# Performance work log

Hardware: AMD Instinct MI355X
Metric: run time of the kernel (lower is better)

## Reference

```python
import jax, jax.numpy as jnp
from jax import lax
import numpy as np

B, N, J, NI, D = 2, 2048, 24, 9, 3
CD, HID = 16, 128
SOFT_BLEND = 20.0
MAX_STEPS, CVG = 50, 1e-5
INIT_BONES = np.array([0, 1, 2, 4, 5, 16, 17, 18, 19])


def _mlp(params, x):
    h = x
    for W, b in params[:-1]:
        h = jax.nn.softplus(h @ W + b)
    W, b = params[-1]
    return h @ W + b


def _broyden(g, x0, J_inv0):
    # x0: [P,3,1], J_inv0: [P,3,3]; fixed MAX_STEPS iterations, track best iterate
    gx = g(x0)
    err0 = jnp.linalg.norm(gx, axis=(1, 2))
    state = (x0, gx, J_inv0, -(J_inv0 @ gx), x0, err0)

    def body(i, st):
        x, gx, Jinv, upd, bx, berr = st
        dx = upd
        x = x + dx
        gx_new = g(x)
        dgx = gx_new - gx
        vT = jnp.swapaxes(dx, -2, -1) @ Jinv            # [P,1,3]
        a = dx - Jinv @ dgx                              # [P,3,1]
        b = vT @ dgx + 1e-6                              # [P,1,1]
        Jinv = Jinv + (a / b) @ vT                       # rank-1 Broyden update
        upd = -(Jinv @ gx_new)
        err = jnp.linalg.norm(gx_new, axis=(1, 2))
        better = err < berr
        bx = jnp.where(better[:, None, None], x, bx)
        berr = jnp.where(better, err, berr)
        return (x, gx_new, Jinv, upd, bx, berr)

    st = lax.fori_loop(0, MAX_STEPS, body, state)
    return st[4], st[5] < CVG


def setup_inputs():
    key = jax.random.key(0)
    ks = jax.random.split(key, 24)
    xd = 0.5 * jax.random.normal(ks[0], (B, N, D), jnp.float32)
    cond_latent = jax.random.normal(ks[1], (B, CD), jnp.float32)
    # near-identity invertible bone transforms
    R = jnp.eye(3, dtype=jnp.float32) + 0.1 * jax.random.normal(ks[2], (B, J, 3, 3), jnp.float32)
    t = 0.1 * jax.random.normal(ks[3], (B, J, 3), jnp.float32)
    tfs = jnp.zeros((B, J, 4, 4), jnp.float32)
    tfs = tfs.at[..., :3, :3].set(R).at[..., :3, 3].set(t).at[..., 3, 3].set(1.0)

    def w(k, fi, fo):
        return jax.random.normal(k, (fi, fo), jnp.float32) / np.sqrt(fi)

    din = D + CD
    inp = dict(xd=xd, cond_latent=cond_latent, tfs=tfs)
    dims_lbs = [(din, HID), (HID, HID), (HID, HID), (HID, J)]
    dims_disp = [(din, HID), (HID, HID), (HID, HID), (HID, D)]
    for i, (fi, fo) in enumerate(dims_lbs):
        inp[f"lbs_w{i}"] = w(ks[4 + i], fi, fo)
        inp[f"lbs_b{i}"] = jnp.zeros((fo,), jnp.float32)
    for i, (fi, fo) in enumerate(dims_disp):
        inp[f"disp_w{i}"] = w(ks[10 + i], fi, fo)
        inp[f"disp_b{i}"] = jnp.zeros((fo,), jnp.float32)
    return inp


def _forward(xd, cond_latent, tfs, lbs, disp):
    P = B * N
    xd_f = xd.reshape(P, D)
    cond_f = jnp.broadcast_to(cond_latent[:, None], (B, N, CD)).reshape(P, CD)
    tfs_f = jnp.broadcast_to(tfs[:, None], (B, N, J, 4, 4)).reshape(P, J, 4, 4)

    # __init: inverse-skin xd with one-hot weights at each init bone -> [P, NI, 3]
    xd_h = jnp.concatenate([xd_f, jnp.ones((P, 1), xd.dtype)], -1)
    xc_init = jnp.einsum('pnij,pj->pni', jnp.linalg.inv(tfs_f[:, INIT_BONES]), xd_h)[..., :3]

    PI = P * NI
    cond_e = jnp.repeat(cond_f, NI, axis=0)       # [PI, CD]
    tfs_e = jnp.repeat(tfs_f, NI, axis=0)         # [PI, J, 4, 4]
    xd_tgt = jnp.repeat(xd_f, NI, axis=0)         # [PI, 3]
    x0 = xc_init.reshape(PI, D)

    def fwd_skin(xc, lbs_p, cond_p, tfs_p):
        w = jax.nn.softmax(SOFT_BLEND * _mlp(lbs_p, jnp.concatenate([xc, cond_p], -1)), -1)
        xh = jnp.concatenate([xc, jnp.ones_like(xc[:, :1])], -1)
        return jnp.einsum('pn,pnij,pj->pi', w, tfs_p, xh)[:, :3]

    def fwd_skin_pt(x, c, t, lbs_p):
        w = jax.nn.softmax(SOFT_BLEND * _mlp(lbs_p, jnp.concatenate([x, c])))
        xh = jnp.concatenate([x, jnp.ones((1,), x.dtype)])
        return jnp.einsum('n,nij,j->i', w, t, xh)[:3]

    def gradient(xc, lbs_p, cond_p, tfs_p):
        # per-point 3x3 Jacobian of forward skinning wrt canonical point
        f = lambda x, c, t: fwd_skin_pt(x, c, t, lbs_p)
        return jax.vmap(jax.jacfwd(f), in_axes=(0, 0, 0))(xc, cond_p, tfs_p)

    # stop-gradient copies for the no-grad broyden search (torch.no_grad block)
    sg = lax.stop_gradient
    lbs_sg = [(sg(W), sg(b)) for W, b in lbs]
    cond_sg, tfs_sg, xdt_sg = sg(cond_e), sg(tfs_e), sg(xd_tgt)

    J_inv0 = jnp.linalg.inv(gradient(sg(x0), lbs_sg, cond_sg, tfs_sg))

    def g_ng(x):  # x: [PI,3,1]
        return (fwd_skin(x[..., 0], lbs_sg, cond_sg, tfs_sg) - xdt_sg)[..., None]

    x_opt, valid = _broyden(g_ng, sg(x0)[..., None], J_inv0)
    xc_opt = sg(x_opt[..., 0])

    # implicit-differentiation correction (eval_mode=False path)
    xd_opt = fwd_skin(xc_opt, lbs, cond_e, tfs_e)
    grad_inv = jnp.linalg.inv(gradient(xc_opt, lbs, cond_e, tfs_e))
    corr = jnp.einsum('pij,pj->pi', -sg(grad_inv), xd_opt - sg(xd_opt))
    xc = xc_opt + corr

    # __query_cano: beta displacement network
    xc = xc + _mlp(disp, jnp.concatenate([xc, cond_e], -1))
    return xc.reshape(B, N, NI, D), valid.reshape(B, N, NI)


def reference(xd, cond_latent, tfs, lbs_w0, lbs_b0, lbs_w1, lbs_b1, lbs_w2, lbs_b2, lbs_w3, lbs_b3, disp_w0, disp_b0, disp_w1, disp_b1, disp_w2, disp_b2, disp_w3, disp_b3):
    lbs = [(lbs_w0, lbs_b0), (lbs_w1, lbs_b1), (lbs_w2, lbs_b2), (lbs_w3, lbs_b3)]
    disp = [(disp_w0, disp_b0), (disp_w1, disp_b1), (disp_w2, disp_b2), (disp_w3, disp_b3)]
    return _forward(xd, cond_latent, tfs, lbs, disp)
```

## Files before the change

### kernel.cpp

```cpp
#include <hip/hip_runtime.h>
#include <hip/hip_bf16.h>
#include <math.h>

#define NB 2
#define NN 2048
#define NJ 24
#define NIB 9
#define NCD 16
#define NHID 128
#define NP (NB * NN)
#define NPI (NP * NIB)
#define NBSTRIDE (NN * NIB)
#define SBLEND 20.0f
#define CVG_EPS 1e-5f
#define MAX_STEPS 50

#define HSTR 129
#define INSTRD 21
#define LSTR 25

static __device__ __forceinline__ float softplusf(float x) {
    return fmaxf(x, 0.0f) + log1pf(expf(-fabsf(x)));
}
static __device__ __forceinline__ float sigmoidf(float x) {
    return 1.0f / (1.0f + expf(-x));
}
static __device__ __forceinline__ int bone_of(int ib) {
    return (ib < 3) ? ib : ((ib < 5) ? ib + 1 : ib + 11);
}

template <int K>
static __device__ __forceinline__ void mv_acc32(const float* __restrict__ Wp, const float* inrow,
                                                int jb, float* acc) {
#pragma unroll 4
    for (int k = 0; k < K; k++) {
        float h = inrow[k];
        const float* wk = Wp + k * NHID + jb;
#pragma unroll
        for (int jj = 0; jj < 32; jj++) acc[jj] = fmaf(h, wk[jj], acc[jj]);
    }
}

template <int K, int LDIN>
static __device__ __forceinline__ void val_layer(const float* __restrict__ Wp,
                                                 const float* __restrict__ bp,
                                                 const float* inbase, float (*Hs)[HSTR], int r,
                                                 int jb, bool prebar) {
    float acc[32];
#pragma unroll
    for (int jj = 0; jj < 32; jj++) acc[jj] = bp[jb + jj];
    mv_acc32<K>(Wp, inbase + r * LDIN, jb, acc);
    if (prebar) __syncthreads();
#pragma unroll
    for (int jj = 0; jj < 32; jj++) Hs[r][jb + jj] = softplusf(acc[jj]);
    __syncthreads();
}

template <int K, int LDIN>
static __device__ __forceinline__ void jac_layer(const float* __restrict__ Wp,
                                                 const float* __restrict__ bp,
                                                 const float* inbase, float (*Hs)[HSTR], int r,
                                                 int jb, bool prebar) {
    const bool isval = (r < 16);
    const int p = r & 15;
    float acc[32];
#pragma unroll
    for (int jj = 0; jj < 32; jj++) acc[jj] = isval ? bp[jb + jj] : 0.0f;
    mv_acc32<K>(Wp, inbase + r * LDIN, jb, acc);
    if (prebar) __syncthreads();
#pragma unroll
    for (int jj = 0; jj < 32; jj++) Hs[r][jb + jj] = acc[jj];
    __syncthreads();
    float zv[32];
    if (!isval) {
#pragma unroll
        for (int jj = 0; jj < 32; jj++) zv[jj] = Hs[p][jb + jj];
    }
    __syncthreads();
    if (isval) {
#pragma unroll
        for (int jj = 0; jj < 32; jj++) Hs[r][jb + jj] = softplusf(acc[jj]);
    } else {
#pragma unroll
        for (int jj = 0; jj < 32; jj++) Hs[r][jb + jj] = sigmoidf(zv[jj]) * acc[jj];
    }
    __syncthreads();
}

template <int NC, int LDW, bool JAC>
static __device__ __forceinline__ void logit_layer(const float* __restrict__ Wp,
                                                   const float* __restrict__ bp,
                                                   const float* inbase, float (*Lgs)[LSTR], int r,
                                                   int wid) {
    const int jb = wid * NC;
    const bool isval = (!JAC) || (r < 16);
    float acc[NC];
#pragma unroll
    for (int jj = 0; jj < NC; jj++) acc[jj] = isval ? bp[jb + jj] : 0.0f;
#pragma unroll 4
    for (int k = 0; k < NHID; k++) {
        float h = inbase[r * HSTR + k];
        const float* wk = Wp + k * LDW + jb;
#pragma unroll
        for (int jj = 0; jj < NC; jj++) acc[jj] = fmaf(h, wk[jj], acc[jj]);
    }
#pragma unroll
    for (int jj = 0; jj < NC; jj++) Lgs[r][jb + jj] = acc[jj];
    __syncthreads();
}

__global__ __launch_bounds__(256) void kernel_fused(
    const float* __restrict__ xd, const float* __restrict__ cond, const float* __restrict__ tfs,
    const float* __restrict__ lw0, const float* __restrict__ lb0,
    const float* __restrict__ lw1, const float* __restrict__ lb1,
    const float* __restrict__ lw2, const float* __restrict__ lb2,
    const float* __restrict__ lw3, const float* __restrict__ lb3,
    const float* __restrict__ dw0, const float* __restrict__ db0,
    const float* __restrict__ dw1, const float* __restrict__ db1,
    const float* __restrict__ dw2, const float* __restrict__ db2,
    const float* __restrict__ dw3, const float* __restrict__ db3,
    float* __restrict__ out) {
    __shared__ float sIN[64][INSTRD];
    __shared__ float sH[64][HSTR];
    __shared__ float sLg[64][LSTR];
    __shared__ float sTm[NJ * 12];
    __shared__ int sFlag;

    const int tid = threadIdx.x;
    const int r = tid & 63;
    const int wid = __builtin_amdgcn_readfirstlane(tid >> 6);
    const int jb = wid * 32;
    const int pi0 = blockIdx.x * 64;
    const int b = pi0 / NBSTRIDE;
    const int pi = pi0 + r;

    for (int t = tid; t < NJ * 12; t += 256) {
        int j = t / 12, rc = t % 12;
        sTm[t] = tfs[(size_t)(b * NJ + j) * 16 + rc];
    }
    if (tid >= 16 && tid < 64) {
        const int d = (tid >> 4) - 1;
#pragma unroll
        for (int k = 0; k < 19; k++) sIN[tid][k] = (k == d) ? 1.0f : 0.0f;
    }
    if (tid < 16) {
#pragma unroll
        for (int cc = 0; cc < NCD; cc++) sIN[tid][3 + cc] = cond[b * NCD + cc];
    }

    float x0_ = 0, x1_ = 0, x2_ = 0, g0 = 0, g1 = 0, g2 = 0;
    float Ji0 = 0, Ji1 = 0, Ji2 = 0, Ji3 = 0, Ji4 = 0, Ji5 = 0, Ji6 = 0, Ji7 = 0, Ji8 = 0;
    float u0 = 0, u1 = 0, u2 = 0, bx0 = 0, bx1 = 0, bx2 = 0, berr = 0;
    float tx = 0, ty = 0, tz = 0;
    if (tid < 64) {
        const int pp = pi / NIB;
        tx = xd[pp * 3 + 0]; ty = xd[pp * 3 + 1]; tz = xd[pp * 3 + 2];
    }

#pragma unroll 1
    for (int pass = 0; pass < 4; ++pass) {
        __syncthreads();
        if ((tid >> 4) == pass) {
            const int p = tid & 15;
            const int ib = pi % NIB;
            const int bone = bone_of(ib);
            const float* T = tfs + (size_t)(b * NJ + bone) * 16;
            float r00 = T[0], r01 = T[1], r02 = T[2], t0 = T[3];
            float r10 = T[4], r11 = T[5], r12 = T[6], t1 = T[7];
            float r20 = T[8], r21 = T[9], r22 = T[10], t2 = T[11];
            float det = r00 * (r11 * r22 - r12 * r21) - r01 * (r10 * r22 - r12 * r20) +
                        r02 * (r10 * r21 - r11 * r20);
            float rd = 1.0f / det;
            float i00 = (r11 * r22 - r12 * r21) * rd, i01 = -(r01 * r22 - r02 * r21) * rd,
                  i02 = (r01 * r12 - r02 * r11) * rd;
            float i10 = -(r10 * r22 - r12 * r20) * rd, i11 = (r00 * r22 - r02 * r20) * rd,
                  i12 = -(r00 * r12 - r02 * r10) * rd;
            float i20 = (r10 * r21 - r11 * r20) * rd, i21 = -(r00 * r21 - r01 * r20) * rd,
                  i22 = (r00 * r11 - r01 * r10) * rd;
            float vx = tx - t0, vy = ty - t1, vz = tz - t2;
            x0_ = i00 * vx + i01 * vy + i02 * vz;
            x1_ = i10 * vx + i11 * vy + i12 * vz;
            x2_ = i20 * vx + i21 * vy + i22 * vz;
            sIN[p][0] = x0_; sIN[p][1] = x1_; sIN[p][2] = x2_;
        }
        __syncthreads();

        jac_layer<19, INSTRD>(lw0, lb0, &sIN[0][0], sH, r, jb, false);
        jac_layer<NHID, HSTR>(lw1, lb1, &sH[0][0], sH, r, jb, true);
        jac_layer<NHID, HSTR>(lw2, lb2, &sH[0][0], sH, r, jb, true);
        logit_layer<6, NJ, true>(lw3, lb3, &sH[0][0], sLg, r, wid);

        if ((tid >> 4) == pass) {
            const int p = tid & 15;
            float mx = -1e30f;
#pragma unroll
            for (int j = 0; j < NJ; j++) mx = fmaxf(mx, SBLEND * sLg[p][j]);
            float S = 0.0f;
#pragma unroll
            for (int j = 0; j < NJ; j++) S += expf(SBLEND * sLg[p][j] - mx);
            const float invS = 1.0f / S;
            float d0 = 0, d1 = 0, d2 = 0;
#pragma unroll
            for (int j = 0; j < NJ; j++) {
                float sj = expf(SBLEND * sLg[p][j] - mx) * invS;
                d0 += sj * (SBLEND * sLg[16 + p][j]);
                d1 += sj * (SBLEND * sLg[32 + p][j]);
                d2 += sj * (SBLEND * sLg[48 + p][j]);
            }
            float f0 = 0, f1 = 0, f2 = 0;
            float J00 = 0, J01 = 0, J02 = 0, J10 = 0, J11 = 0, J12 = 0, J20 = 0, J21 = 0,
                  J22 = 0;
#pragma unroll
            for (int j = 0; j < NJ; j++) {
                float sj = expf(SBLEND * sLg[p][j] - mx) * invS;
                float uj0 = SBLEND * sLg[16 + p][j], uj1 = SBLEND * sLg[32 + p][j],
                      uj2 = SBLEND * sLg[48 + p][j];
                float sd0 = sj * (uj0 - d0), sd1 = sj * (uj1 - d1), sd2 = sj * (uj2 - d2);
                const float* M = &sTm[j * 12];
                float y0 = M[0] * x0_ + M[1] * x1_ + M[2] * x2_ + M[3];
                float y1 = M[4] * x0_ + M[5] * x1_ + M[6] * x2_ + M[7];
                float y2 = M[8] * x0_ + M[9] * x1_ + M[10] * x2_ + M[11];
                f0 += sj * y0; f1 += sj * y1; f2 += sj * y2;
                J00 += sd0 * y0 + sj * M[0]; J01 += sd1 * y0 + sj * M[1]; J02 += sd2 * y0 + sj * M[2];
                J10 += sd0 * y1 + sj * M[4]; J11 += sd1 * y1 + sj * M[5]; J12 += sd2 * y1 + sj * M[6];
                J20 += sd0 * y2 + sj * M[8]; J21 += sd1 * y2 + sj * M[9]; J22 += sd2 * y2 + sj * M[10];
            }
            g0 = f0 - tx; g1 = f1 - ty; g2 = f2 - tz;
            float detJ = J00 * (J11 * J22 - J12 * J21) - J01 * (J10 * J22 - J12 * J20) +
                         J02 * (J10 * J21 - J11 * J20);
            float rdJ = 1.0f / detJ;
            Ji0 = (J11 * J22 - J12 * J21) * rdJ; Ji1 = -(J01 * J22 - J02 * J21) * rdJ;
            Ji2 = (J01 * J12 - J02 * J11) * rdJ;
            Ji3 = -(J10 * J22 - J12 * J20) * rdJ; Ji4 = (J00 * J22 - J02 * J20) * rdJ;
            Ji5 = -(J00 * J12 - J02 * J10) * rdJ;
            Ji6 = (J10 * J21 - J11 * J20) * rdJ; Ji7 = -(J00 * J21 - J01 * J20) * rdJ;
            Ji8 = (J00 * J11 - J01 * J10) * rdJ;
            u0 = -(Ji0 * g0 + Ji1 * g1 + Ji2 * g2);
            u1 = -(Ji3 * g0 + Ji4 * g1 + Ji5 * g2);
            u2 = -(Ji6 * g0 + Ji7 * g1 + Ji8 * g2);
            berr = sqrtf(g0 * g0 + g1 * g1 + g2 * g2);
            bx0 = x0_; bx1 = x1_; bx2 = x2_;
        }
    }

    if (tid < 64) {
#pragma unroll
        for (int cc = 0; cc < NCD; cc++) sIN[tid][3 + cc] = cond[b * NCD + cc];
    }

#pragma unroll 1
    for (int it = 0; it < MAX_STEPS; ++it) {
        float dx0 = 0, dx1 = 0, dx2 = 0;
        if (tid < 64) {
            dx0 = u0; dx1 = u1; dx2 = u2;
            x0_ += dx0; x1_ += dx1; x2_ += dx2;
            sIN[tid][0] = x0_; sIN[tid][1] = x1_; sIN[tid][2] = x2_;
        }
        __syncthreads();

        val_layer<19, INSTRD>(lw0, lb0, &sIN[0][0], sH, r, jb, false);
        val_layer<NHID, HSTR>(lw1, lb1, &sH[0][0], sH, r, jb, true);
        val_layer<NHID, HSTR>(lw2, lb2, &sH[0][0], sH, r, jb, true);
        logit_layer<6, NJ, false>(lw3, lb3, &sH[0][0], sLg, r, wid);

        if (tid < 64) {
            float mx = -1e30f;
#pragma unroll
            for (int j = 0; j < NJ; j++) mx = fmaxf(mx, SBLEND * sLg[r][j]);
            float S = 0.0f;
#pragma unroll
            for (int j = 0; j < NJ; j++) {
                float e = expf(SBLEND * sLg[r][j] - mx);
                sLg[r][j] = e;
                S += e;
            }
            const float invS = 1.0f / S;
            float f0 = 0, f1 = 0, f2 = 0;
#pragma unroll
            for (int j = 0; j < NJ; j++) {
                float sj = sLg[r][j] * invS;
                const float* M = &sTm[j * 12];
                f0 += sj * (M[0] * x0_ + M[1] * x1_ + M[2] * x2_ + M[3]);
                f1 += sj * (M[4] * x0_ + M[5] * x1_ + M[6] * x2_ + M[7]);
                f2 += sj * (M[8] * x0_ + M[9] * x1_ + M[10] * x2_ + M[11]);
            }
            float gn0 = f0 - tx, gn1 = f1 - ty, gn2 = f2 - tz;
            float dg0 = gn0 - g0, dg1 = gn1 - g1, dg2 = gn2 - g2;
            float Jd0 = Ji0 * dg0 + Ji1 * dg1 + Ji2 * dg2;
            float Jd1 = Ji3 * dg0 + Ji4 * dg1 + Ji5 * dg2;
            float Jd2 = Ji6 * dg0 + Ji7 * dg1 + Ji8 * dg2;
            float v0 = dx0 * Ji0 + dx1 * Ji3 + dx2 * Ji6;
            float v1 = dx0 * Ji1 + dx1 * Ji4 + dx2 * Ji7;
            float v2 = dx0 * Ji2 + dx1 * Ji5 + dx2 * Ji8;
            float a0 = dx0 - Jd0, a1 = dx1 - Jd1, a2 = dx2 - Jd2;
            float bden = v0 * dg0 + v1 * dg1 + v2 * dg2 + 1e-6f;
            float s0 = a0 / bden, s1 = a1 / bden, s2 = a2 / bden;
            Ji0 += s0 * v0; Ji1 += s0 * v1; Ji2 += s0 * v2;
            Ji3 += s1 * v0; Ji4 += s1 * v1; Ji5 += s1 * v2;
            Ji6 += s2 * v0; Ji7 += s2 * v1; Ji8 += s2 * v2;
            u0 = -(Ji0 * gn0 + Ji1 * gn1 + Ji2 * gn2);
            u1 = -(Ji3 * gn0 + Ji4 * gn1 + Ji5 * gn2);
            u2 = -(Ji6 * gn0 + Ji7 * gn1 + Ji8 * gn2);
            float err = sqrtf(gn0 * gn0 + gn1 * gn1 + gn2 * gn2);
            if (err < berr) { berr = err; bx0 = x0_; bx1 = x1_; bx2 = x2_; }
            g0 = gn0; g1 = gn1; g2 = gn2;
            int allc = __all(berr < CVG_EPS);
            if (tid == 0) sFlag = allc;
        }
        __syncthreads();
        if (sFlag) break;
    }

    if (tid < 64) {
        sIN[tid][0] = bx0; sIN[tid][1] = bx1; sIN[tid][2] = bx2;
    }
    __syncthreads();

    val_layer<19, INSTRD>(dw0, db0, &sIN[0][0], sH, r, jb, false);
    val_layer<NHID, HSTR>(dw1, db1, &sH[0][0], sH, r, jb, true);
    val_layer<NHID, HSTR>(dw2, db2, &sH[0][0], sH, r, jb, true);

    if (tid < 64) {
        float a0 = db3[0], a1 = db3[1], a2 = db3[2];
#pragma unroll 4
        for (int k = 0; k < NHID; k++) {
            float h = sH[tid][k];
            a0 = fmaf(h, dw3[k * 3 + 0], a0);
            a1 = fmaf(h, dw3[k * 3 + 1], a1);
            a2 = fmaf(h, dw3[k * 3 + 2], a2);
        }
        out[pi * 3 + 0] = bx0 + a0;
        out[pi * 3 + 1] = bx1 + a1;
        out[pi * 3 + 2] = bx2 + a2;
        out[3 * NPI + pi] = (berr < CVG_EPS) ? 1.0f : 0.0f;
    }
}

extern "C" void kernel_launch(void* const* d_in, const int* in_sizes, int n_in,
                              void* d_out, int out_size, void* d_ws, size_t ws_size,
                              hipStream_t stream) {
    (void)in_sizes; (void)n_in; (void)out_size; (void)d_ws; (void)ws_size;
    const float* xd   = (const float*)d_in[0];
    const float* cond = (const float*)d_in[1];
    const float* tfs  = (const float*)d_in[2];
    const float* lw0 = (const float*)d_in[3];  const float* lb0 = (const float*)d_in[4];
    const float* lw1 = (const float*)d_in[5];  const float* lb1 = (const float*)d_in[6];
    const float* lw2 = (const float*)d_in[7];  const float* lb2 = (const float*)d_in[8];
    const float* lw3 = (const float*)d_in[9];  const float* lb3 = (const float*)d_in[10];
    const float* dw0 = (const float*)d_in[11]; const float* db0 = (const float*)d_in[12];
    const float* dw1 = (const float*)d_in[13]; const float* db1 = (const float*)d_in[14];
    const float* dw2 = (const float*)d_in[15]; const float* db2 = (const float*)d_in[16];
    const float* dw3 = (const float*)d_in[17]; const float* db3 = (const float*)d_in[18];
    float* out = (float*)d_out;

    kernel_fused<<<NPI / 64, 256, 0, stream>>>(xd, cond, tfs, lw0, lb0, lw1, lb1, lw2, lb2,
                                               lw3, lb3, dw0, db0, dw1, db1, dw2, db2, dw3, db3,
                                               out);
}
```

Before: 1.499 ms.

## Split Broyden solve into block pass plus compacted straggler pass

Splits the fused kernel into three launches. The first runs Broyden per 64-row block with 512 threads and exits early once at most 16 rows remain unconverged. It then writes the solver state of unconverged rows into a compacted workspace list through an atomic counter. A second kernel packs those stragglers densely and finishes their remaining iterations, and a third kernel runs the displacement MLP. This aims to stop whole blocks from iterating for a few slow rows and to double the threads per block, at the cost of workspace traffic, extra launches and a memset.

New measurement: 1.247 ms. 16.8% less time.

```diff
diff --git a/kernel.cpp b/kernel.cpp
--- a/kernel.cpp
+++ b/kernel.cpp
@@ -1,5 +1,4 @@
 #include <hip/hip_runtime.h>
-#include <hip/hip_bf16.h>
 #include <math.h>
 
 #define NB 2
@@ -14,11 +13,17 @@
 #define SBLEND 20.0f
 #define CVG_EPS 1e-5f
 #define MAX_STEPS 50
+#define THRESH 16
 
 #define HSTR 129
 #define INSTRD 21
 #define LSTR 25
 
+#define WS_BX 4
+#define WS_BE (4 + 3 * NPI)
+#define WS_META (4 + 4 * NPI)
+#define WS_ST (4 + 5 * NPI)
+
 static __device__ __forceinline__ float softplusf(float x) {
     return fmaxf(x, 0.0f) + log1pf(expf(-fabsf(x)));
 }
@@ -30,14 +35,14 @@
 }
 
 template <int K>
-static __device__ __forceinline__ void mv_acc32(const float* __restrict__ Wp, const float* inrow,
+static __device__ __forceinline__ void mv_acc16(const float* __restrict__ Wp, const float* inrow,
                                                 int jb, float* acc) {
 #pragma unroll 4
     for (int k = 0; k < K; k++) {
         float h = inrow[k];
         const float* wk = Wp + k * NHID + jb;
 #pragma unroll
-        for (int jj = 0; jj < 32; jj++) acc[jj] = fmaf(h, wk[jj], acc[jj]);
+        for (int jj = 0; jj < 16; jj++) acc[jj] = fmaf(h, wk[jj], acc[jj]);
     }
 }
 
@@ -46,13 +51,13 @@
                                                  const float* __restrict__ bp,
                                                  const float* inbase, float (*Hs)[HSTR], int r,
                                                  int jb, bool prebar) {
-    float acc[32];
-#pragma unroll
-    for (int jj = 0; jj < 32; jj++) acc[jj] = bp[jb + jj];
-    mv_acc32<K>(Wp, inbase + r * LDIN, jb, acc);
+    float acc[16];
+#pragma unroll
+    for (int jj = 0; jj < 16; jj++) acc[jj] = bp[jb + jj];
+    mv_acc16<K>(Wp, inbase + r * LDIN, jb, acc);
     if (prebar) __syncthreads();
 #pragma unroll
-    for (int jj = 0; jj < 32; jj++) Hs[r][jb + jj] = softplusf(acc[jj]);
+    for (int jj = 0; jj < 16; jj++) Hs[r][jb + jj] = softplusf(acc[jj]);
     __syncthreads();
 }
 
@@ -63,78 +68,124 @@
                                                  int jb, bool prebar) {
     const bool isval = (r < 16);
     const int p = r & 15;
-    float acc[32];
-#pragma unroll
-    for (int jj = 0; jj < 32; jj++) acc[jj] = isval ? bp[jb + jj] : 0.0f;
-    mv_acc32<K>(Wp, inbase + r * LDIN, jb, acc);
+    float acc[16];
+#pragma unroll
+    for (int jj = 0; jj < 16; jj++) acc[jj] = isval ? bp[jb + jj] : 0.0f;
+    mv_acc16<K>(Wp, inbase + r * LDIN, jb, acc);
     if (prebar) __syncthreads();
 #pragma unroll
-    for (int jj = 0; jj < 32; jj++) Hs[r][jb + jj] = acc[jj];
+    for (int jj = 0; jj < 16; jj++) Hs[r][jb + jj] = acc[jj];
     __syncthreads();
-    float zv[32];
+    float zv[16];
     if (!isval) {
 #pragma unroll
-        for (int jj = 0; jj < 32; jj++) zv[jj] = Hs[p][jb + jj];
+        for (int jj = 0; jj < 16; jj++) zv[jj] = Hs[p][jb + jj];
     }
     __syncthreads();
     if (isval) {
 #pragma unroll
-        for (int jj = 0; jj < 32; jj++) Hs[r][jb + jj] = softplusf(acc[jj]);
+        for (int jj = 0; jj < 16; jj++) Hs[r][jb + jj] = softplusf(acc[jj]);
     } else {
 #pragma unroll
-        for (int jj = 0; jj < 32; jj++) Hs[r][jb + jj] = sigmoidf(zv[jj]) * acc[jj];
+        for (int jj = 0; jj < 16; jj++) Hs[r][jb + jj] = sigmoidf(zv[jj]) * acc[jj];
     }
     __syncthreads();
 }
 
-template <int NC, int LDW, bool JAC>
+template <bool JAC>
 static __device__ __forceinline__ void logit_layer(const float* __restrict__ Wp,
                                                    const float* __restrict__ bp,
                                                    const float* inbase, float (*Lgs)[LSTR], int r,
                                                    int wid) {
-    const int jb = wid * NC;
+    const int jb = wid * 3;
     const bool isval = (!JAC) || (r < 16);
-    float acc[NC];
-#pragma unroll
-    for (int jj = 0; jj < NC; jj++) acc[jj] = isval ? bp[jb + jj] : 0.0f;
+    float acc[3];
+#pragma unroll
+    for (int jj = 0; jj < 3; jj++) acc[jj] = isval ? bp[jb + jj] : 0.0f;
 #pragma unroll 4
     for (int k = 0; k < NHID; k++) {
         float h = inbase[r * HSTR + k];
-        const float* wk = Wp + k * LDW + jb;
-#pragma unroll
-        for (int jj = 0; jj < NC; jj++) acc[jj] = fmaf(h, wk[jj], acc[jj]);
-    }
-#pragma unroll
-    for (int jj = 0; jj < NC; jj++) Lgs[r][jb + jj] = acc[jj];
+        const float* wk = Wp + k * NJ + jb;
+#pragma unroll
+        for (int jj = 0; jj < 3; jj++) acc[jj] = fmaf(h, wk[jj], acc[jj]);
+    }
+#pragma unroll
+    for (int jj = 0; jj < 3; jj++) Lgs[r][jb + jj] = acc[jj];
     __syncthreads();
 }
 
-__global__ __launch_bounds__(256) void kernel_fused(
+static __device__ __forceinline__ void broyden_step(
+    float* sLgRow, const float* sTm, float tx, float ty, float tz,
+    float dx0, float dx1, float dx2,
+    float& x0_, float& x1_, float& x2_, float& g0, float& g1, float& g2,
+    float& Ji0, float& Ji1, float& Ji2, float& Ji3, float& Ji4, float& Ji5,
+    float& Ji6, float& Ji7, float& Ji8,
+    float& u0, float& u1, float& u2,
+    float& bx0, float& bx1, float& bx2, float& berr) {
+    float mx = -1e30f;
+#pragma unroll
+    for (int j = 0; j < NJ; j++) mx = fmaxf(mx, SBLEND * sLgRow[j]);
+    float S = 0.0f;
+#pragma unroll
+    for (int j = 0; j < NJ; j++) {
+        float e = expf(SBLEND * sLgRow[j] - mx);
+        sLgRow[j] = e;
+        S += e;
+    }
+    const float invS = 1.0f / S;
+    float f0 = 0, f1 = 0, f2 = 0;
+#pragma unroll
+    for (int j = 0; j < NJ; j++) {
+        float sj = sLgRow[j] * invS;
+        const float* M = &sTm[j * 12];
+        f0 += sj * (M[0] * x0_ + M[1] * x1_ + M[2] * x2_ + M[3]);
+        f1 += sj * (M[4] * x0_ + M[5] * x1_ + M[6] * x2_ + M[7]);
+        f2 += sj * (M[8] * x0_ + M[9] * x1_ + M[10] * x2_ + M[11]);
+    }
+    float gn0 = f0 - tx, gn1 = f1 - ty, gn2 = f2 - tz;
+    float dg0 = gn0 - g0, dg1 = gn1 - g1, dg2 = gn2 - g2;
+    float Jd0 = Ji0 * dg0 + Ji1 * dg1 + Ji2 * dg2;
+    float Jd1 = Ji3 * dg0 + Ji4 * dg1 + Ji5 * dg2;
+    float Jd2 = Ji6 * dg0 + Ji7 * dg1 + Ji8 * dg2;
+    float v0 = dx0 * Ji0 + dx1 * Ji3 + dx2 * Ji6;
+    float v1 = dx0 * Ji1 + dx1 * Ji4 + dx2 * Ji7;
+    float v2 = dx0 * Ji2 + dx1 * Ji5 + dx2 * Ji8;
+    float a0 = dx0 - Jd0, a1 = dx1 - Jd1, a2 = dx2 - Jd2;
+    float bden = v0 * dg0 + v1 * dg1 + v2 * dg2 + 1e-6f;
+    float s0 = a0 / bden, s1 = a1 / bden, s2 = a2 / bden;
+    Ji0 += s0 * v0; Ji1 += s0 * v1; Ji2 += s0 * v2;
+    Ji3 += s1 * v0; Ji4 += s1 * v1; Ji5 += s1 * v2;
+    Ji6 += s2 * v0; Ji7 += s2 * v1; Ji8 += s2 * v2;
+    u0 = -(Ji0 * gn0 + Ji1 * gn1 + Ji2 * gn2);
+    u1 = -(Ji3 * gn0 + Ji4 * gn1 + Ji5 * gn2);
+    u2 = -(Ji6 * gn0 + Ji7 * gn1 + Ji8 * gn2);
+    float err = sqrtf(gn0 * gn0 + gn1 * gn1 + gn2 * gn2);
+    if (err < berr) { berr = err; bx0 = x0_; bx1 = x1_; bx2 = x2_; }
+    g0 = gn0; g1 = gn1; g2 = gn2;
+}
+
+__global__ __launch_bounds__(512) void kernel_a(
     const float* __restrict__ xd, const float* __restrict__ cond, const float* __restrict__ tfs,
     const float* __restrict__ lw0, const float* __restrict__ lb0,
     const float* __restrict__ lw1, const float* __restrict__ lb1,
     const float* __restrict__ lw2, const float* __restrict__ lb2,
     const float* __restrict__ lw3, const float* __restrict__ lb3,
-    const float* __restrict__ dw0, const float* __restrict__ db0,
-    const float* __restrict__ dw1, const float* __restrict__ db1,
-    const float* __restrict__ dw2, const float* __restrict__ db2,
-    const float* __restrict__ dw3, const float* __restrict__ db3,
-    float* __restrict__ out) {
+    float* __restrict__ ws) {
     __shared__ float sIN[64][INSTRD];
     __shared__ float sH[64][HSTR];
     __shared__ float sLg[64][LSTR];
     __shared__ float sTm[NJ * 12];
-    __shared__ int sFlag;
+    __shared__ int sCnt;
 
     const int tid = threadIdx.x;
     const int r = tid & 63;
     const int wid = __builtin_amdgcn_readfirstlane(tid >> 6);
-    const int jb = wid * 32;
+    const int jb = wid * 16;
     const int pi0 = blockIdx.x * 64;
     const int b = pi0 / NBSTRIDE;
     const int pi = pi0 + r;
 
-    for (int t = tid; t < NJ * 12; t += 256) {
+    for (int t = tid; t < NJ * 12; t += 512) {
         int j = t / 12, rc = t % 12;
         sTm[t] = tfs[(size_t)(b * NJ + j) * 16 + rc];
     }
@@ -160,11 +211,10 @@
 #pragma unroll 1
     for (int pass = 0; pass < 4; ++pass) {
         __syncthreads();
-        if ((tid >> 4) == pass) {
+        if (tid < 64 && (tid >> 4) == pass) {
             const int p = tid & 15;
             const int ib = pi % NIB;
-            const int bone = bone_of(ib);
-            const float* T = tfs + (size_t)(b * NJ + bone) * 16;
+            const float* T = tfs + (size_t)(b * NJ + bone_of(ib)) * 16;
             float r00 = T[0], r01 = T[1], r02 = T[2], t0 = T[3];
             float r10 = T[4], r11 = T[5], r12 = T[6], t1 = T[7];
             float r20 = T[8], r21 = T[9], r22 = T[10], t2 = T[11];
@@ -188,9 +238,9 @@
         jac_layer<19, INSTRD>(lw0, lb0, &sIN[0][0], sH, r, jb, false);
         jac_layer<NHID, HSTR>(lw1, lb1, &sH[0][0], sH, r, jb, true);
         jac_layer<NHID, HSTR>(lw2, lb2, &sH[0][0], sH, r, jb, true);
-        logit_layer<6, NJ, true>(lw3, lb3, &sH[0][0], sLg, r, wid);
-
-        if ((tid >> 4) == pass) {
+        logit_layer<true>(lw3, lb3, &sH[0][0], sLg, r, wid);
+
+        if (tid < 64 && (tid >> 4) == pass) {
             const int p = tid & 15;
             float mx = -1e30f;
 #pragma unroll
@@ -248,6 +298,7 @@
         for (int cc = 0; cc < NCD; cc++) sIN[tid][3 + cc] = cond[b * NCD + cc];
     }
 
+    int itdone = MAX_STEPS;
 #pragma unroll 1
     for (int it = 0; it < MAX_STEPS; ++it) {
         float dx0 = 0, dx1 = 0, dx2 = 0;
@@ -261,58 +312,173 @@
         val_layer<19, INSTRD>(lw0, lb0, &sIN[0][0], sH, r, jb, false);
         val_layer<NHID, HSTR>(lw1, lb1, &sH[0][0], sH, r, jb, true);
         val_layer<NHID, HSTR>(lw2, lb2, &sH[0][0], sH, r, jb, true);
-        logit_layer<6, NJ, false>(lw3, lb3, &sH[0][0], sLg, r, wid);
+        logit_layer<false>(lw3, lb3, &sH[0][0], sLg, r, wid);
 
         if (tid < 64) {
-            float mx = -1e30f;
-#pragma unroll
-            for (int j = 0; j < NJ; j++) mx = fmaxf(mx, SBLEND * sLg[r][j]);
-            float S = 0.0f;
-#pragma unroll
-            for (int j = 0; j < NJ; j++) {
-                float e = expf(SBLEND * sLg[r][j] - mx);
-                sLg[r][j] = e;
-                S += e;
+            broyden_step(&sLg[r][0], sTm, tx, ty, tz, dx0, dx1, dx2,
+                         x0_, x1_, x2_, g0, g1, g2,
+                         Ji0, Ji1, Ji2, Ji3, Ji4, Ji5, Ji6, Ji7, Ji8,
+                         u0, u1, u2, bx0, bx1, bx2, berr);
+            unsigned long long m = __ballot(!(berr < CVG_EPS));
+            if (tid == 0) sCnt = (int)__popcll(m);
+        }
+        __syncthreads();
+        if (sCnt <= THRESH) { itdone = it + 1; break; }
+    }
+
+    if (tid < 64) {
+        ws[WS_BX + pi * 3 + 0] = bx0;
+        ws[WS_BX + pi * 3 + 1] = bx1;
+        ws[WS_BX + pi * 3 + 2] = bx2;
+        ws[WS_BE + pi] = berr;
+        const int remaining = MAX_STEPS - itdone;
+        if (remaining > 0 && !(berr < CVG_EPS)) {
+            int idx = atomicAdd((int*)ws + b, 1);
+            int slot = b * NBSTRIDE + idx;
+            ((int*)ws)[WS_META + slot] = pi | (remaining << 20);
+            float st[15] = {x0_, x1_, x2_, g0, g1, g2, Ji0, Ji1, Ji2, Ji3, Ji4, Ji5, Ji6, Ji7, Ji8};
+#pragma unroll
+            for (int c = 0; c < 15; c++) ws[WS_ST + c * NPI + slot] = st[c];
+        }
+    }
+}
+
+__global__ __launch_bounds__(512) void kernel_b(
+    const float* __restrict__ xd, const float* __restrict__ cond, const float* __restrict__ tfs,
+    const float* __restrict__ lw0, const float* __restrict__ lb0,
+    const float* __restrict__ lw1, const float* __restrict__ lb1,
+    const float* __restrict__ lw2, const float* __restrict__ lb2,
+    const float* __restrict__ lw3, const float* __restrict__ lb3,
+    float* __restrict__ ws) {
+    const int bid = blockIdx.x;
+    const int batch = (bid < 288) ? 0 : 1;
+    const int chunk0 = (bid - batch * 288) * 64;
+    const int S = ((const int*)ws)[batch];
+    if (chunk0 >= S) return;
+
+    __shared__ float sIN[64][INSTRD];
+    __shared__ float sH[64][HSTR];
+    __shared__ float sLg[64][LSTR];
+    __shared__ float sTm[NJ * 12];
+    __shared__ int sCnt;
+
+    const int tid = threadIdx.x;
+    const int r = tid & 63;
+    const int wid = __builtin_amdgcn_readfirstlane(tid >> 6);
+    const int jb = wid * 16;
+
+    for (int t = tid; t < NJ * 12; t += 512) {
+        int j = t / 12, rc = t % 12;
+        sTm[t] = tfs[(size_t)(batch * NJ + j) * 16 + rc];
+    }
+
+    float x0_ = 0, x1_ = 0, x2_ = 0, g0 = 0, g1 = 0, g2 = 0;
+    float Ji0 = 1, Ji1 = 0, Ji2 = 0, Ji3 = 0, Ji4 = 1, Ji5 = 0, Ji6 = 0, Ji7 = 0, Ji8 = 1;
+    float u0 = 0, u1 = 0, u2 = 0, bx0 = 0, bx1 = 0, bx2 = 0, berr = 0;
+    float tx = 0, ty = 0, tz = 0;
+    int pi = -1, itleft = 0;
+    bool realrow = false;
+    if (tid < 64) {
+        const int k = chunk0 + r;
+        realrow = (k < S);
+        if (realrow) {
+            const int slot = batch * NBSTRIDE + k;
+            const int meta = ((const int*)ws)[WS_META + slot];
+            pi = meta & 0xFFFFF;
+            itleft = meta >> 20;
+            x0_ = ws[WS_ST + 0 * NPI + slot]; x1_ = ws[WS_ST + 1 * NPI + slot];
+            x2_ = ws[WS_ST + 2 * NPI + slot];
+            g0 = ws[WS_ST + 3 * NPI + slot]; g1 = ws[WS_ST + 4 * NPI + slot];
+            g2 = ws[WS_ST + 5 * NPI + slot];
+            Ji0 = ws[WS_ST + 6 * NPI + slot]; Ji1 = ws[WS_ST + 7 * NPI + slot];
+            Ji2 = ws[WS_ST + 8 * NPI + slot];
+            Ji3 = ws[WS_ST + 9 * NPI + slot]; Ji4 = ws[WS_ST + 10 * NPI + slot];
+            Ji5 = ws[WS_ST + 11 * NPI + slot];
+            Ji6 = ws[WS_ST + 12 * NPI + slot]; Ji7 = ws[WS_ST + 13 * NPI + slot];
+            Ji8 = ws[WS_ST + 14 * NPI + slot];
+            u0 = -(Ji0 * g0 + Ji1 * g1 + Ji2 * g2);
+            u1 = -(Ji3 * g0 + Ji4 * g1 + Ji5 * g2);
+            u2 = -(Ji6 * g0 + Ji7 * g1 + Ji8 * g2);
+            bx0 = ws[WS_BX + pi * 3 + 0]; bx1 = ws[WS_BX + pi * 3 + 1];
+            bx2 = ws[WS_BX + pi * 3 + 2];
+            berr = ws[WS_BE + pi];
+            const int pp = pi / NIB;
+            tx = xd[pp * 3 + 0]; ty = xd[pp * 3 + 1]; tz = xd[pp * 3 + 2];
+        }
+#pragma unroll
+        for (int cc = 0; cc < NCD; cc++) sIN[tid][3 + cc] = cond[batch * NCD + cc];
+        sIN[tid][0] = 0; sIN[tid][1] = 0; sIN[tid][2] = 0;
+    }
+
+#pragma unroll 1
+    for (int it = 0; it < MAX_STEPS; ++it) {
+        bool active = false;
+        float dx0 = 0, dx1 = 0, dx2 = 0;
+        if (tid < 64) {
+            active = realrow && (itleft > 0) && !(berr < CVG_EPS);
+            if (active) {
+                dx0 = u0; dx1 = u1; dx2 = u2;
+                x0_ += dx0; x1_ += dx1; x2_ += dx2;
             }
-            const float invS = 1.0f / S;
-            float f0 = 0, f1 = 0, f2 = 0;
-#pragma unroll
-            for (int j = 0; j < NJ; j++) {
-                float sj = sLg[r][j] * invS;
-                const float* M = &sTm[j * 12];
-                f0 += sj * (M[0] * x0_ + M[1] * x1_ + M[2] * x2_ + M[3]);
-                f1 += sj * (M[4] * x0_ + M[5] * x1_ + M[6] * x2_ + M[7]);
-                f2 += sj * (M[8] * x0_ + M[9] * x1_ + M[10] * x2_ + M[11]);
+            sIN[tid][0] = x0_; sIN[tid][1] = x1_; sIN[tid][2] = x2_;
+        }
+        __syncthreads();
+
+        val_layer<19, INSTRD>(lw0, lb0, &sIN[0][0], sH, r, jb, false);
+        val_layer<NHID, HSTR>(lw1, lb1, &sH[0][0], sH, r, jb, true);
+        val_layer<NHID, HSTR>(lw2, lb2, &sH[0][0], sH, r, jb, true);
+        logit_layer<false>(lw3, lb3, &sH[0][0], sLg, r, wid);
+
+        if (tid < 64) {
+            if (active) {
+                broyden_step(&sLg[r][0], sTm, tx, ty, tz, dx0, dx1, dx2,
+                             x0_, x1_, x2_, g0, g1, g2,
+                             Ji0, Ji1, Ji2, Ji3, Ji4, Ji5, Ji6, Ji7, Ji8,
+                             u0, u1, u2, bx0, bx1, bx2, berr);
+                itleft--;
             }
-            float gn0 = f0 - tx, gn1 = f1 - ty, gn2 = f2 - tz;
-            float dg0 = gn0 - g0, dg1 = gn1 - g1, dg2 = gn2 - g2;
-            float Jd0 = Ji0 * dg0 + Ji1 * dg1 + Ji2 * dg2;
-            float Jd1 = Ji3 * dg0 + Ji4 * dg1 + Ji5 * dg2;
-            float Jd2 = Ji6 * dg0 + Ji7 * dg1 + Ji8 * dg2;
-            float v0 = dx0 * Ji0 + dx1 * Ji3 + dx2 * Ji6;
-            float v1 = dx0 * Ji1 + dx1 * Ji4 + dx2 * Ji7;
-            float v2 = dx0 * Ji2 + dx1 * Ji5 + dx2 * Ji8;
-            float a0 = dx0 - Jd0, a1 = dx1 - Jd1, a2 = dx2 - Jd2;
-            float bden = v0 * dg0 + v1 * dg1 + v2 * dg2 + 1e-6f;
-            float s0 = a0 / bden, s1 = a1 / bden, s2 = a2 / bden;
-            Ji0 += s0 * v0; Ji1 += s0 * v1; Ji2 += s0 * v2;
-            Ji3 += s1 * v0; Ji4 += s1 * v1; Ji5 += s1 * v2;
-            Ji6 += s2 * v0; Ji7 += s2 * v1; Ji8 += s2 * v2;
-            u0 = -(Ji0 * gn0 + Ji1 * gn1 + Ji2 * gn2);
-            u1 = -(Ji3 * gn0 + Ji4 * gn1 + Ji5 * gn2);
-            u2 = -(Ji6 * gn0 + Ji7 * gn1 + Ji8 * gn2);
-            float err = sqrtf(gn0 * gn0 + gn1 * gn1 + gn2 * gn2);
-            if (err < berr) { berr = err; bx0 = x0_; bx1 = x1_; bx2 = x2_; }
-            g0 = gn0; g1 = gn1; g2 = gn2;
-            int allc = __all(berr < CVG_EPS);
-            if (tid == 0) sFlag = allc;
+            unsigned long long m =
+                __ballot(realrow && (itleft > 0) && !(berr < CVG_EPS));
+            if (tid == 0) sCnt = (int)__popcll(m);
         }
         __syncthreads();
-        if (sFlag) break;
-    }
-
+        if (sCnt == 0) break;
+    }
+
+    if (tid < 64 && realrow) {
+        ws[WS_BX + pi * 3 + 0] = bx0;
+        ws[WS_BX + pi * 3 + 1] = bx1;
+        ws[WS_BX + pi * 3 + 2] = bx2;
+        ws[WS_BE + pi] = berr;
+    }
+}
+
+__global__ __launch_bounds__(512) void kernel_c(
+    const float* __restrict__ cond,
+    const float* __restrict__ dw0, const float* __restrict__ db0,
+    const float* __restrict__ dw1, const float* __restrict__ db1,
+    const float* __restrict__ dw2, const float* __restrict__ db2,
+    const float* __restrict__ dw3, const float* __restrict__ db3,
+    const float* __restrict__ ws, float* __restrict__ out) {
+    __shared__ float sIN[64][INSTRD];
+    __shared__ float sH[64][HSTR];
+
+    const int tid = threadIdx.x;
+    const int r = tid & 63;
+    const int wid = __builtin_amdgcn_readfirstlane(tid >> 6);
+    const int jb = wid * 16;
+    const int pi0 = blockIdx.x * 64;
+    const int b = pi0 / NBSTRIDE;
+    const int pi = pi0 + r;
+
+    float bx0 = 0, bx1 = 0, bx2 = 0, berr = 0;
     if (tid < 64) {
+        bx0 = ws[WS_BX + pi * 3 + 0]; bx1 = ws[WS_BX + pi * 3 + 1];
+        bx2 = ws[WS_BX + pi * 3 + 2];
+        berr = ws[WS_BE + pi];
         sIN[tid][0] = bx0; sIN[tid][1] = bx1; sIN[tid][2] = bx2;
+#pragma unroll
+        for (int cc = 0; cc < NCD; cc++) sIN[tid][3 + cc] = cond[b * NCD + cc];
     }
     __syncthreads();
 
@@ -339,7 +505,7 @@
 extern "C" void kernel_launch(void* const* d_in, const int* in_sizes, int n_in,
                               void* d_out, int out_size, void* d_ws, size_t ws_size,
                               hipStream_t stream) {
-    (void)in_sizes; (void)n_in; (void)out_size; (void)d_ws; (void)ws_size;
+    (void)in_sizes; (void)n_in; (void)out_size; (void)ws_size;
     const float* xd   = (const float*)d_in[0];
     const float* cond = (const float*)d_in[1];
     const float* tfs  = (const float*)d_in[2];
@@ -351,9 +517,14 @@
     const float* dw1 = (const float*)d_in[13]; const float* db1 = (const float*)d_in[14];
     const float* dw2 = (const float*)d_in[15]; const float* db2 = (const float*)d_in[16];
     const float* dw3 = (const float*)d_in[17]; const float* db3 = (const float*)d_in[18];
+    float* ws = (float*)d_ws;
     float* out = (float*)d_out;
 
-    kernel_fused<<<NPI / 64, 256, 0, stream>>>(xd, cond, tfs, lw0, lb0, lw1, lb1, lw2, lb2,
-                                               lw3, lb3, dw0, db0, dw1, db1, dw2, db2, dw3, db3,
-                                               out);
-}
+    hipMemsetAsync(d_ws, 0, 16, stream);
+    kernel_a<<<NPI / 64, 512, 0, stream>>>(xd, cond, tfs, lw0, lb0, lw1, lb1, lw2, lb2,
+                                           lw3, lb3, ws);
+    kernel_b<<<576, 512, 0, stream>>>(xd, cond, tfs, lw0, lb0, lw1, lb1, lw2, lb2,
+                                      lw3, lb3, ws);
+    kernel_c<<<NPI / 64, 512, 0, stream>>>(cond, dw0, db0, dw1, db1, dw2, db2, dw3, db3,
+                                           ws, out);
+}
```
